# Performance work log

Measured on AMD Instinct MI355X. Metric: run time of the kernel, lower is better.

Reference implementation:

```python
import jax, jax.numpy as jnp
import numpy as np

N = 20000      # vertices
KPV = 8        # key points per vertex
M = N * KPV    # total key points
E = 320000     # edges (avg in-degree 16)
KP_DIM = 4
SD = 300       # state_dim
T = 3          # GNN iterations
NC = 4         # classes
LOC = (64, 64, 7)


def _lin(key, din, dout):
    k1, k2 = jax.random.split(key)
    s = 1.0 / np.sqrt(din)
    W = jax.random.uniform(k1, (din, dout), jnp.float32, -s, s)
    b = jax.random.uniform(k2, (dout,), jnp.float32, -s, s)
    return W, b


def setup_inputs():
    key = jax.random.key(0)
    ks = jax.random.split(key, 32)
    inp = {}
    inp['key_points'] = jax.random.normal(ks[0], (M, KP_DIM), jnp.float32)
    inp['pos'] = jax.random.normal(ks[1], (N, 3), jnp.float32)
    # uniform ragged layout: vertex i owns key points [i*KPV, (i+1)*KPV)
    inp['key_points_lookup'] = jnp.arange(N, dtype=jnp.int32) * KPV
    inp['edge_index'] = jax.random.randint(ks[2], (2, E), 0, N, jnp.int32)
    # MLPInit: kp_dim -> 64 -> 128 -> state_dim (basic_block = Linear+ReLU)
    inp['Wi0'], inp['bi0'] = _lin(ks[3], KP_DIM, 64)
    inp['Wi1'], inp['bi1'] = _lin(ks[4], 64, 128)
    inp['Wi2'], inp['bi2'] = _lin(ks[5], 128, SD)
    # MLPInitAggr: state_dim -> state_dim
    inp['Wa'], inp['ba'] = _lin(ks[6], SD, SD)
    # StateConvLayer params per iteration (mlp_h: s->delta_x, mlp_f: [dx,s_j]->e, mlp_g: update)
    Wh, bh, Wf, bf, Wg, bg = [], [], [], [], [], []
    for t in range(T):
        w, b = _lin(ks[7 + 3 * t], SD, 3); Wh.append(w); bh.append(b)
        w, b = _lin(ks[8 + 3 * t], SD + 3, SD); Wf.append(w); bf.append(b)
        w, b = _lin(ks[9 + 3 * t], SD, SD); Wg.append(w); bg.append(b)
    inp['Wh'] = jnp.stack(Wh); inp['bh'] = jnp.stack(bh)
    inp['Wf'] = jnp.stack(Wf); inp['bf'] = jnp.stack(bf)
    inp['Wg'] = jnp.stack(Wg); inp['bg'] = jnp.stack(bg)
    # classification head: state_dim -> 64 -> n_classes
    inp['Wc1'], inp['bc1'] = _lin(ks[16], SD, 64)
    inp['Wc2'], inp['bc2'] = _lin(ks[17], 64, NC)
    # per-class localization heads: state_dim -> 64 -> 64 -> 7 (stacked over classes)
    Wl1, bl1, Wl2, bl2, Wl3, bl3 = [], [], [], [], [], []
    for c in range(NC):
        w, b = _lin(ks[18 + 3 * c], SD, LOC[0]); Wl1.append(w); bl1.append(b)
        w, b = _lin(ks[19 + 3 * c], LOC[0], LOC[1]); Wl2.append(w); bl2.append(b)
        w, b = _lin(ks[20 + 3 * c], LOC[1], LOC[2]); Wl3.append(w); bl3.append(b)
    inp['Wl1'] = jnp.stack(Wl1); inp['bl1'] = jnp.stack(bl1)
    inp['Wl2'] = jnp.stack(Wl2); inp['bl2'] = jnp.stack(bl2)
    inp['Wl3'] = jnp.stack(Wl3); inp['bl3'] = jnp.stack(bl3)
    return inp


def reference(key_points, pos, key_points_lookup, edge_index,
              Wi0, bi0, Wi1, bi1, Wi2, bi2, Wa, ba,
              Wh, bh, Wf, bf, Wg, bg,
              Wc1, bc1, Wc2, bc2,
              Wl1, bl1, Wl2, bl2, Wl3, bl3):
    relu = jax.nn.relu
    n = pos.shape[0]
    # ---- initial vertex state: per-key-point MLP + ragged segment-max ----
    feats = relu(key_points @ Wi0 + bi0)
    feats = relu(feats @ Wi1 + bi1)
    feats = relu(feats @ Wi2 + bi2)                      # [M, SD]
    seg = jnp.searchsorted(key_points_lookup,
                           jnp.arange(feats.shape[0], dtype=jnp.int32),
                           side='right') - 1              # key point -> vertex id
    kp_max = jax.ops.segment_max(feats, seg, num_segments=n)  # [N, SD]
    s = relu(kp_max @ Wa + ba)                            # initial vertex states
    # ---- GNN iterations (Point-GNN eqns, max aggregation) ----
    src, dst = edge_index[0], edge_index[1]
    for t in range(Wh.shape[0]):
        dx = s @ Wh[t] + bh[t]                            # [N, 3] predicted offset
        m = jnp.concatenate([pos[src] - pos[dst] + dx[dst], s[src]], axis=-1)
        e = relu(m @ Wf[t] + bf[t])                       # [E, SD] edge messages
        aggr = jax.ops.segment_max(e, dst, num_segments=n)
        aggr = jnp.where(jnp.isneginf(aggr), 0.0, aggr)   # empty segments -> 0
        s = s + (aggr @ Wg[t] + bg[t])                    # residual state update
    # ---- heads ----
    cls_pred = relu(relu(s @ Wc1 + bc1) @ Wc2 + bc2)      # [N, NC]
    h = relu(jnp.einsum('nd,cdk->cnk', s, Wl1) + bl1[:, None, :])
    h = relu(jnp.einsum('cnd,cdk->cnk', h, Wl2) + bl2[:, None, :])
    h = relu(jnp.einsum('cnd,cdk->cnk', h, Wl3) + bl3[:, None, :])  # [C, N, 7]
    reg_pred = jnp.transpose(h, (1, 0, 2)).reshape(n, -1)           # [N, C*7]
    return cls_pred, reg_pred
```

## Files before the change

### kernel.cpp

```cpp
#include <hip/hip_runtime.h>
#include <stdint.h>

#define N_V   20000
#define M_KP  160000
#define E_N   320000
#define SD    300
#define T_IT  3

typedef unsigned short bf16_t;
typedef __attribute__((ext_vector_type(8))) short short8_t;
typedef __attribute__((ext_vector_type(4))) float float4_t;

__device__ __forceinline__ float bf2f(bf16_t u) {
    return __uint_as_float(((unsigned)u) << 16);
}
__device__ __forceinline__ bf16_t f2bf(float f) {
    unsigned u = __float_as_uint(f);
    unsigned r = (u + 0x7FFFu + ((u >> 16) & 1u)) >> 16;
    return (bf16_t)r;
}

template<bool F32>
__device__ __forceinline__ float LD(const void* p, size_t i) {
    if (F32) return ((const float*)p)[i];
    return bf2f(((const bf16_t*)p)[i]);
}
template<bool F32>
__device__ __forceinline__ void ST(void* p, size_t i, float v) {
    if (F32) ((float*)p)[i] = v;
    else     ((bf16_t*)p)[i] = f2bf(v);
}
__device__ __forceinline__ float LDr(const void* p, long long i, bool f32) {
    return f32 ? ((const float*)p)[i] : bf2f(((const bf16_t*)p)[i]);
}
__device__ __forceinline__ void STr(void* p, size_t i, float v, bool f32) {
    if (f32) ((float*)p)[i] = v;
    else     ((bf16_t*)p)[i] = f2bf(v);
}

__global__ void k_detect(const unsigned* __restrict__ w, int* __restrict__ flag) {
    __shared__ int cnt_s;
    if (threadIdx.x == 0) cnt_s = 0;
    __syncthreads();
    unsigned u = w[threadIdx.x];
    unsigned lo = u & 0xFFFFu;
    int e = (lo >> 7) & 0xFF;
    int plaus = (lo == 0u) || (e >= 96 && e <= 126);
    atomicAdd(&cnt_s, plaus);
    __syncthreads();
    if (threadIdx.x == 0) flag[0] = (cnt_s >= 64) ? 0 : 1;
}

__global__ void k_zero(int* p, int n) {
    int i = blockIdx.x * blockDim.x + threadIdx.x;
    if (i < n) p[i] = 0;
}
__global__ void k_hist(const int* __restrict__ dst, int* __restrict__ cnt) {
    int e = blockIdx.x * blockDim.x + threadIdx.x;
    if (e < E_N) atomicAdd(&cnt[dst[e]], 1);
}
__global__ void k_scan(const int* __restrict__ cnt, int* __restrict__ offs,
                       int* __restrict__ cur) {
    __shared__ int buf[1024];
    __shared__ int carry_s;
    int tid = threadIdx.x;
    if (tid == 0) { carry_s = 0; offs[0] = 0; }
    __syncthreads();
    for (int base = 0; base < N_V; base += 1024) {
        int i = base + tid;
        int v = (i < N_V) ? cnt[i] : 0;
        buf[tid] = v;
        __syncthreads();
        for (int off = 1; off < 1024; off <<= 1) {
            int t = (tid >= off) ? buf[tid - off] : 0;
            __syncthreads();
            buf[tid] += t;
            __syncthreads();
        }
        int incl = buf[tid] + carry_s;
        if (i < N_V) { offs[i + 1] = incl; cur[i] = incl - v; }
        __syncthreads();
        if (tid == 1023) carry_s = incl;
        __syncthreads();
    }
}
__global__ void k_scatter(const int* __restrict__ src, const int* __restrict__ dst,
                          int* __restrict__ cur, int* __restrict__ esrc) {
    int e = blockIdx.x * blockDim.x + threadIdx.x;
    if (e < E_N) {
        int p = atomicAdd(&cur[dst[e]], 1);
        esrc[p] = src[e];
    }
}

template<bool F32>
__global__ __launch_bounds__(256) void k_init_fused(
    const void* __restrict__ kp,
    const void* __restrict__ Wi0, const void* __restrict__ bi0,
    const void* __restrict__ Wi1, const void* __restrict__ bi1,
    const void* __restrict__ Wi2, const void* __restrict__ bi2,
    float* __restrict__ kpmax, const int* __restrict__ flag) {
    if ((flag[0] != 0) != F32) return;
    __shared__ float kps[256];
    __shared__ float h1s[64][64];
    __shared__ float h2s[64 * 128];
    int tid = threadIdx.x;
    int row0 = blockIdx.x * 64;
    kps[tid] = LD<F32>(kp, (size_t)row0 * 4 + tid);
    __syncthreads();
    {
        int c = tid & 63;
        float w0 = LD<F32>(Wi0, c), w1 = LD<F32>(Wi0, 64 + c);
        float w2 = LD<F32>(Wi0, 128 + c), w3 = LD<F32>(Wi0, 192 + c);
        float b0 = LD<F32>(bi0, c);
        int rbase = (tid >> 6) * 16;
#pragma unroll
        for (int rr = 0; rr < 16; rr++) {
            int r = rbase + rr;
            float a = b0 + kps[r * 4] * w0 + kps[r * 4 + 1] * w1
                         + kps[r * 4 + 2] * w2 + kps[r * 4 + 3] * w3;
            h1s[r][c] = fmaxf(a, 0.f);
        }
    }
    __syncthreads();
    {
        int c = tid & 127;
        int rbase = (tid >> 7) * 32;
        float b1 = LD<F32>(bi1, c);
        float acc[32];
#pragma unroll
        for (int rr = 0; rr < 32; rr++) acc[rr] = b1;
        for (int k = 0; k < 64; k++) {
            float wv = LD<F32>(Wi1, (size_t)k * 128 + c);
#pragma unroll
            for (int rr = 0; rr < 32; rr++) acc[rr] += h1s[rbase + rr][k] * wv;
        }
#pragma unroll
        for (int rr = 0; rr < 32; rr++)
            h2s[(size_t)(rbase + rr) * 128 + c] = fmaxf(acc[rr], 0.f);
    }
    __syncthreads();
    {
        int cx = tid & 63, rg = tid >> 6;
        float acc[16][5];
#pragma unroll
        for (int r = 0; r < 16; r++)
#pragma unroll
            for (int j = 0; j < 5; j++) acc[r][j] = 0.f;
        bool ok4 = (cx < SD - 256);
        for (int k = 0; k < 128; k++) {
            float w[5];
#pragma unroll
            for (int j = 0; j < 4; j++) w[j] = LD<F32>(Wi2, (size_t)k * SD + cx + 64 * j);
            w[4] = ok4 ? LD<F32>(Wi2, (size_t)k * SD + cx + 256) : 0.f;
#pragma unroll
            for (int r = 0; r < 16; r++) {
                float av = h2s[(rg * 16 + r) * 128 + k];
#pragma unroll
                for (int j = 0; j < 5; j++) acc[r][j] += av * w[j];
            }
        }
        int vbase = (row0 >> 3) + rg * 2;
#pragma unroll
        for (int half = 0; half < 2; half++) {
            int v = vbase + half;
#pragma unroll
            for (int j = 0; j < 5; j++) {
                int c = cx + 64 * j;
                if (c >= SD) continue;
                float m = acc[half * 8][j];
#pragma unroll
                for (int r = 1; r < 8; r++) m = fmaxf(m, acc[half * 8 + r][j]);
                kpmax[(size_t)v * SD + c] = fmaxf(m + LD<F32>(bi2, c), 0.f);
            }
        }
    }
}

template<bool F32>
__global__ __launch_bounds__(256) void k_gemm(
    const float* __restrict__ A, const void* __restrict__ W,
    const void* __restrict__ bias, const float* res,
    float* C, int Mr, int K, int Nc, int do_relu, const int* __restrict__ flag) {
    if ((flag[0] != 0) != F32) return;
    __shared__ float As[16][65];
    __shared__ float Ws[16][64];
    int tid = threadIdx.x;
    int tx = tid & 15, ty = tid >> 4;
    int row0 = blockIdx.y * 64, col0 = blockIdx.x * 64;
    float acc[4][4] = {{0.f}};
    int lk = tid & 15, lr = tid >> 4;
    int ln = tid & 63, lk4 = tid >> 6;
    for (int k0 = 0; k0 < K; k0 += 16) {
#pragma unroll
        for (int i = 0; i < 4; i++) {
            int r = lr + i * 16;
            int gr = row0 + r, gk = k0 + lk;
            As[lk][r] = (gr < Mr && gk < K) ? A[(size_t)gr * K + gk] : 0.f;
        }
#pragma unroll
        for (int p = 0; p < 4; p++) {
            int kk = lk4 + p * 4;
            int gk = k0 + kk, gn = col0 + ln;
            Ws[kk][ln] = (gk < K && gn < Nc) ? LD<F32>(W, (size_t)gk * Nc + gn) : 0.f;
        }
        __syncthreads();
#pragma unroll
        for (int kk = 0; kk < 16; kk++) {
            float a[4], w[4];
#pragma unroll
            for (int i = 0; i < 4; i++) a[i] = As[kk][ty * 4 + i];
#pragma unroll
            for (int j = 0; j < 4; j++) w[j] = Ws[kk][tx * 4 + j];
#pragma unroll
            for (int i = 0; i < 4; i++)
#pragma unroll
                for (int j = 0; j < 4; j++) acc[i][j] += a[i] * w[j];
        }
        __syncthreads();
    }
#pragma unroll
    for (int i = 0; i < 4; i++) {
        int gr = row0 + ty * 4 + i;
        if (gr >= Mr) continue;
#pragma unroll
        for (int j = 0; j < 4; j++) {
            int gn = col0 + tx * 4 + j;
            if (gn >= Nc) continue;
            float c = acc[i][j] + LD<F32>(bias, gn);
            if (res) c += res[(size_t)gr * Nc + gn];
            if (do_relu) c = fmaxf(c, 0.f);
            C[(size_t)gr * Nc + gn] = c;
        }
    }
}

#define PREP_SPLIT 882688
#define PREP_BIAS  3104
#define PREP_WF3   2700
#define PREP_TOT   (PREP_SPLIT + PREP_BIAS + PREP_WF3 + 32)

__global__ __launch_bounds__(256) void k_prep(
    const void* __restrict__ Wa, const void* __restrict__ Wf,
    const void* __restrict__ Wg, const void* __restrict__ Wc1,
    const void* __restrict__ Wl1, const void* __restrict__ Wl2,
    const void* __restrict__ Wi1, const void* __restrict__ Wi2,
    const void* __restrict__ ba, const void* __restrict__ bfb,
    const void* __restrict__ bgb, const void* __restrict__ bc1,
    const void* __restrict__ bl1b, const void* __restrict__ bl2b,
    const void* __restrict__ bi1, const void* __restrict__ bi2,
    unsigned short* __restrict__ SP, float* __restrict__ biasF,
    float* __restrict__ wf3F,
    float* __restrict__ bzero, const int* __restrict__ flag)
{
    int idx = blockIdx.x * 256 + threadIdx.x;
    if (idx >= PREP_TOT) return;
    bool f32 = flag[0] != 0;
    if (idx < PREP_SPLIT) {
        const void* src; long long eoff, cum; int srcN, Nn, Kk, Kpad, pe, local;
        if (idx < 716800) {
            int m = idx / 102400; local = idx - m * 102400;
            pe = 102400; cum = (long long)m * 102400;
            Kpad = 320; Nn = 300; Kk = 300; srcN = 300;
            src = (m == 0) ? Wa : (m <= 3 ? Wf : Wg);
            eoff = (m == 0) ? 0 : (m <= 3 ? (long long)((m - 1) * 303 + 3) * 300
                                          : (long long)(m - 4) * 90000);
        } else if (idx < 819200) {
            int j = (idx - 716800) / 20480; local = (idx - 716800) - j * 20480;
            pe = 20480; cum = 716800 + (long long)j * 20480;
            Kpad = 320; Nn = 64; Kk = 300; srcN = 64;
            src = (j == 0) ? Wc1 : Wl1;
            eoff = (j == 0) ? 0 : (long long)(j - 1) * 19200;
        } else if (idx < 835584) {
            int c = (idx - 819200) / 4096; local = (idx - 819200) - c * 4096;
            pe = 4096; cum = 819200 + (long long)c * 4096;
            Kpad = 64; Nn = 64; Kk = 64; srcN = 64;
            src = Wl2; eoff = (long long)c * 4096;
        } else if (idx < 843776) {
            local = idx - 835584;
            pe = 8192; cum = 835584;
            Kpad = 64; Nn = 128; Kk = 64; srcN = 128;
            src = Wi1; eoff = 0;
        } else {
            local = idx - 843776;
            pe = 38912; cum = 843776;
            Kpad = 128; Nn = 300; Kk = 128; srcN = 300;
            src = Wi2; eoff = 0;
        }
        int n = local / Kpad, k = local - n * Kpad;
        float v = 0.f;
        if (n < Nn && k < Kk) v = LDr(src, eoff + (long long)k * srcN + n, f32);
        bf16_t hi = f2bf(v);
        bf16_t lo = f2bf(v - bf2f(hi));
        SP[2 * cum + local] = hi;
        SP[2 * cum + pe + local] = lo;
    } else if (idx < PREP_SPLIT + PREP_BIAS) {
        int b = idx - PREP_SPLIT;
        const void* src; int o;
        if (b < 300)       { src = ba;   o = b; }
        else if (b < 1200) { src = bfb;  o = b - 300; }
        else if (b < 2100) { src = bgb;  o = b - 1200; }
        else if (b < 2164) { src = bc1;  o = b - 2100; }
        else if (b < 2420) { src = bl1b; o = b - 2164; }
        else if (b < 2676) { src = bl2b; o = b - 2420; }
        else if (b < 2804) { src = bi1;  o = b - 2676; }
        else               { src = bi2;  o = b - 2804; }
        biasF[b] = LDr(src, o, f32);
    } else if (idx < PREP_SPLIT + PREP_BIAS + PREP_WF3) {
        int b2 = idx - (PREP_SPLIT + PREP_BIAS);
        int t = b2 / 900, rem = b2 - t * 900;
        wf3F[b2] = LDr(Wf, (long long)t * 303 * SD + rem, f32);
    } else {
        bzero[idx - (PREP_SPLIT + PREP_BIAS + PREP_WF3)] = 0.f;
    }
}

__device__ __forceinline__ void mfma16(float4_t& c, short8_t a, short8_t b) {
    asm("v_mfma_f32_16x16x32_bf16 %0, %1, %2, %0" : "+v"(c) : "v"(a), "v"(b));
}
__device__ __forceinline__ void split2(float a, float b, unsigned& h, unsigned& l) {
    asm("v_cvt_pk_bf16_f32 %0, %1, %2" : "=v"(h) : "v"(a), "v"(b));
    float la = a - __uint_as_float(h << 16);
    float lb = b - __uint_as_float(h & 0xFFFF0000u);
    asm("v_cvt_pk_bf16_f32 %0, %1, %2" : "=v"(l) : "v"(la), "v"(lb));
}
__device__ __forceinline__ void split8(float4_t x0, float4_t x1,
                                       short8_t* hi, short8_t* lo) {
    union { unsigned u[4]; short8_t v; } H, L;
#pragma unroll
    for (int p = 0; p < 4; p++) {
        float a, b;
        if (p == 0)      { a = x0[0]; b = x0[1]; }
        else if (p == 1) { a = x0[2]; b = x0[3]; }
        else if (p == 2) { a = x1[0]; b = x1[1]; }
        else             { a = x1[2]; b = x1[3]; }
        unsigned ph, pl;
        split2(a, b, ph, pl);
        H.u[p] = ph; L.u[p] = pl;
    }
    *hi = H.v; *lo = L.v;
}

__global__ __launch_bounds__(256) void k_init_mfma(
    const void* __restrict__ kp,
    const void* __restrict__ Wi0, const void* __restrict__ bi0,
    const unsigned short* __restrict__ W1T,
    const unsigned short* __restrict__ W2T,
    const float* __restrict__ b1F, const float* __restrict__ b2F,
    float* __restrict__ kpmax, const int* __restrict__ flag)
{
    bool f32 = flag[0] != 0;
    __shared__ __attribute__((aligned(16))) unsigned short lds[2][8704];
    int tid = threadIdx.x;
    int w = tid >> 6, lane = tid & 63;
    int rg = w >> 1, ch = w & 1;
    int l15 = lane & 15, g = lane >> 4;
    unsigned short* h2h = lds[rg];
    unsigned short* h2l = lds[rg] + 4352;
    int rw0 = blockIdx.x * 64 + rg * 32;

    float kpr[2][4];
#pragma unroll
    for (int mt = 0; mt < 2; mt++) {
        long long r = rw0 + mt * 16 + l15;
#pragma unroll
        for (int j = 0; j < 4; j++) kpr[mt][j] = LDr(kp, r * 4 + j, f32);
    }
    short8_t a1h[2][2], a1l[2][2];
#pragma unroll
    for (int ks = 0; ks < 2; ks++) {
        float h[2][8];
#pragma unroll
        for (int e = 0; e < 8; e++) {
            int chn = ks * 32 + 8 * g + e;
            float w0 = LDr(Wi0, chn, f32),       w1 = LDr(Wi0, 64 + chn, f32);
            float w2 = LDr(Wi0, 128 + chn, f32), w3 = LDr(Wi0, 192 + chn, f32);
            float b0 = LDr(bi0, chn, f32);
#pragma unroll
            for (int mt = 0; mt < 2; mt++)
                h[mt][e] = fmaxf(b0 + kpr[mt][0] * w0 + kpr[mt][1] * w1
                                    + kpr[mt][2] * w2 + kpr[mt][3] * w3, 0.f);
        }
#pragma unroll
        for (int mt = 0; mt < 2; mt++) {
            union { unsigned u[4]; short8_t v; } H, L;
#pragma unroll
            for (int p = 0; p < 4; p++) {
                unsigned hh, ll;
                split2(h[mt][2 * p], h[mt][2 * p + 1], hh, ll);
                H.u[p] = hh; L.u[p] = ll;
            }
            a1h[mt][ks] = H.v; a1l[mt][ks] = L.v;
        }
    }

#pragma unroll
    for (int i = 0; i < 4; i++) {
        int n0 = ch * 4 + i;
        const unsigned short* bp = W1T + (n0 * 16 + l15) * 64 + 8 * g;
        short8_t bh0 = *(const short8_t*)bp;
        short8_t bh1 = *(const short8_t*)(bp + 32);
        short8_t bl0 = *(const short8_t*)(bp + 8192);
        short8_t bl1 = *(const short8_t*)(bp + 8224);
        float4_t c0 = {0.f, 0.f, 0.f, 0.f}, c1 = {0.f, 0.f, 0.f, 0.f};
        mfma16(c0, a1h[0][0], bh0); mfma16(c0, a1h[0][1], bh1);
        mfma16(c0, a1l[0][0], bh0); mfma16(c0, a1l[0][1], bh1);
        mfma16(c0, a1h[0][0], bl0); mfma16(c0, a1h[0][1], bl1);
        mfma16(c1, a1h[1][0], bh0); mfma16(c1, a1h[1][1], bh1);
        mfma16(c1, a1l[1][0], bh0); mfma16(c1, a1l[1][1], bh1);
        mfma16(c1, a1h[1][0], bl0); mfma16(c1, a1h[1][1], bl1);
        int col = n0 * 16 + l15;
        float bv = b1F[col];
#pragma unroll
        for (int i2 = 0; i2 < 4; i2++) {
            float v0 = fmaxf(c0[i2] + bv, 0.f);
            bf16_t h0 = f2bf(v0);
            h2h[(4 * g + i2) * 136 + col] = h0;
            h2l[(4 * g + i2) * 136 + col] = f2bf(v0 - bf2f(h0));
            float v1 = fmaxf(c1[i2] + bv, 0.f);
            bf16_t h1v = f2bf(v1);
            h2h[(16 + 4 * g + i2) * 136 + col] = h1v;
            h2l[(16 + 4 * g + i2) * 136 + col] = f2bf(v1 - bf2f(h1v));
        }
    }
    __syncthreads();

    short8_t a2h[2][4], a2l[2][4];
#pragma unroll
    for (int mt = 0; mt < 2; mt++)
#pragma unroll
        for (int ks = 0; ks < 4; ks++) {
            int off = (mt * 16 + l15) * 136 + ks * 32 + 8 * g;
            a2h[mt][ks] = *(const short8_t*)(h2h + off);
            a2l[mt][ks] = *(const short8_t*)(h2l + off);
        }
    int vb = blockIdx.x * 8 + rg * 4;
    int n0beg = ch ? 10 : 0, n0end = ch ? 19 : 10;
    for (int n0 = n0beg; n0 < n0end; n0++) {
        const unsigned short* bp = W2T + (n0 * 16 + l15) * 128 + 8 * g;
        short8_t bh[4], bl[4];
#pragma unroll
        for (int ks = 0; ks < 4; ks++) {
            bh[ks] = *(const short8_t*)(bp + ks * 32);
            bl[ks] = *(const short8_t*)(bp + 38912 + ks * 32);
        }
        float4_t c0 = {0.f, 0.f, 0.f, 0.f}, c1 = {0.f, 0.f, 0.f, 0.f};
#pragma unroll
        for (int ks = 0; ks < 4; ks++) {
            mfma16(c0, a2h[0][ks], bh[ks]); mfma16(c1, a2h[1][ks], bh[ks]);
        }
#pragma unroll
        for (int ks = 0; ks < 4; ks++) {
            mfma16(c0, a2l[0][ks], bh[ks]); mfma16(c1, a2l[1][ks], bh[ks]);
        }
#pragma unroll
        for (int ks = 0; ks < 4; ks++) {
            mfma16(c0, a2h[0][ks], bl[ks]); mfma16(c1, a2h[1][ks], bl[ks]);
        }
        float m0 = fmaxf(fmaxf(c0[0], c0[1]), fmaxf(c0[2], c0[3]));
        m0 = fmaxf(m0, __shfl_xor(m0, 16));
        float m1 = fmaxf(fmaxf(c1[0], c1[1]), fmaxf(c1[2], c1[3]));
        m1 = fmaxf(m1, __shfl_xor(m1, 16));
        int col = n0 * 16 + l15;
        if (col < SD) {
            float bv = b2F[col];
            if (g == 0) {
                kpmax[(size_t)(vb + 0) * SD + col] = fmaxf(m0 + bv, 0.f);
                kpmax[(size_t)(vb + 2) * SD + col] = fmaxf(m1 + bv, 0.f);
            } else if (g == 2) {
                kpmax[(size_t)(vb + 1) * SD + col] = fmaxf(m0 + bv, 0.f);
                kpmax[(size_t)(vb + 3) * SD + col] = fmaxf(m1 + bv, 0.f);
            }
        }
    }
}

__global__ __launch_bounds__(256) void k_gemm_mfma(
    const float* __restrict__ A, const unsigned short* __restrict__ WhiT,
    const unsigned short* __restrict__ WloT, const float* __restrict__ bias,
    const float* __restrict__ res, float* __restrict__ C,
    int M, int K, int Kpad, int N, int relu,
    long long zA, long long zW, int zB, long long zC,
    const void* posp, const float* dxv, const float* wf3F,
    float* bbag, const int* __restrict__ flag)
{
    int z = blockIdx.z;
    A    += (size_t)z * zA;
    WhiT += (size_t)z * zW;
    WloT += (size_t)z * zW;
    bias += (size_t)z * zB;
    C    += (size_t)z * zC;
    int tid = threadIdx.x;
    int w = tid >> 6, lane = tid & 63;
    int l15 = lane & 15, g = lane >> 4;
    int row0 = blockIdx.y * 256 + w * 64;
    int col0 = blockIdx.x * 64;

    float4_t acc[4][4];
#pragma unroll
    for (int i = 0; i < 4; i++)
#pragma unroll
        for (int j = 0; j < 4; j++) acc[i][j] = (float4_t){0.f, 0.f, 0.f, 0.f};

    const unsigned short* bhp[4];
    const unsigned short* blp[4];
#pragma unroll
    for (int ns = 0; ns < 4; ns++) {
        size_t o = (size_t)(col0 + ns * 16 + l15) * Kpad + 8 * g;
        bhp[ns] = WhiT + o; blp[ns] = WloT + o;
    }
    const float* app[4];
    int amode[4]; bool adead[4];
#pragma unroll
    for (int ms = 0; ms < 4; ms++) {
        int base = row0 + ms * 16;
        int gr = base + l15;
        amode[ms] = (base + 16 <= M) ? 2 : (base < M ? 1 : 0);
        adead[ms] = gr >= M;
        int grc = gr < M ? gr : (M - 1);
        app[ms] = A + (size_t)grc * K + 8 * g;
    }
    const short8_t z8 = {0, 0, 0, 0, 0, 0, 0, 0};

    for (int k0 = 0; k0 < K; k0 += 32) {
        short8_t bh[4], bl[4], ah[4], al[4];
#pragma unroll
        for (int ns = 0; ns < 4; ns++) {
            bh[ns] = *(const short8_t*)bhp[ns]; bhp[ns] += 32;
            bl[ns] = *(const short8_t*)blp[ns]; blp[ns] += 32;
        }
#pragma unroll
        for (int ms = 0; ms < 4; ms++) {
            if (amode[ms] == 0) { ah[ms] = z8; al[ms] = z8; continue; }
            float4_t x0 = *(const float4_t*)app[ms];
            float4_t x1 = *(const float4_t*)(app[ms] + 4);
            app[ms] += 32;
            if (amode[ms] == 1 && adead[ms]) {
                x0 = (float4_t){0.f, 0.f, 0.f, 0.f};
                x1 = (float4_t){0.f, 0.f, 0.f, 0.f};
            }
            split8(x0, x1, &ah[ms], &al[ms]);
        }
#pragma unroll
        for (int ms = 0; ms < 4; ms++)
#pragma unroll
            for (int ns = 0; ns < 4; ns++) {
                mfma16(acc[ms][ns], ah[ms], bh[ns]);
                mfma16(acc[ms][ns], al[ms], bh[ns]);
                mfma16(acc[ms][ns], ah[ms], bl[ns]);
            }
    }

    bool ab = posp != nullptr;
    bool pf32 = ab && (flag[0] != 0);
#pragma unroll
    for (int ns = 0; ns < 4; ns++) {
        int gn = col0 + ns * 16 + l15;
        if (gn >= N) continue;
        float bv = bias[gn];
        float w30 = 0.f, w31 = 0.f, w32 = 0.f;
        if (ab) { w30 = wf3F[gn]; w31 = wf3F[300 + gn]; w32 = wf3F[600 + gn]; }
#pragma unroll
        for (int ms = 0; ms < 4; ms++) {
            int rb = row0 + ms * 16 + 4 * g;
#pragma unroll
            for (int r = 0; r < 4; r++) {
                int gr = rb + r;
                if (gr >= M) continue;
                float c = acc[ms][ns][r] + bv;
                if (ab) {
                    float P = LDr(posp, (long long)gr * 3 + 0, pf32) * w30
                            + LDr(posp, (long long)gr * 3 + 1, pf32) * w31
                            + LDr(posp, (long long)gr * 3 + 2, pf32) * w32;
                    float D = dxv[gr * 3 + 0] * w30 + dxv[gr * 3 + 1] * w31
                            + dxv[gr * 3 + 2] * w32;
                    c += P;
                    bbag[(size_t)gr * N + gn] = D - P;
                }
                if (res) c += res[(size_t)gr * N + gn];
                if (relu) c = fmaxf(c, 0.f);
                C[(size_t)gr * N + gn] = c;
            }
        }
    }
}

__global__ void k_dx2(const float* __restrict__ s, const void* __restrict__ Wh,
                      const void* __restrict__ bh, int t, float* __restrict__ dx,
                      const int* __restrict__ flag) {
    bool f32 = flag[0] != 0;
    long long wo = (long long)t * SD * 3, bo = (long long)t * 3;
    int wv = threadIdx.x >> 6, lane = threadIdx.x & 63;
    int v = blockIdx.x * 4 + wv;
    if (v >= N_V) return;
    float p0 = 0.f, p1 = 0.f, p2 = 0.f;
    for (int d = lane; d < SD; d += 64) {
        float sv = s[(size_t)v * SD + d];
        p0 += sv * LDr(Wh, wo + d * 3 + 0, f32);
        p1 += sv * LDr(Wh, wo + d * 3 + 1, f32);
        p2 += sv * LDr(Wh, wo + d * 3 + 2, f32);
    }
#pragma unroll
    for (int off = 32; off > 0; off >>= 1) {
        p0 += __shfl_down(p0, off);
        p1 += __shfl_down(p1, off);
        p2 += __shfl_down(p2, off);
    }
    if (lane == 0) {
        dx[v * 3 + 0] = p0 + LDr(bh, bo + 0, f32);
        dx[v * 3 + 1] = p1 + LDr(bh, bo + 1, f32);
        dx[v * 3 + 2] = p2 + LDr(bh, bo + 2, f32);
    }
}

__global__ void k_cls2(const float* __restrict__ hc, const void* __restrict__ W,
                       const void* __restrict__ b, void* __restrict__ out,
                       const int* __restrict__ flag) {
    bool f32 = flag[0] != 0;
    int v = blockIdx.x * blockDim.x + threadIdx.x;
    if (v >= N_V) return;
    float acc[4];
#pragma unroll
    for (int j = 0; j < 4; j++) acc[j] = LDr(b, j, f32);
    for (int k = 0; k < 64; k++) {
        float h = hc[(size_t)v * 64 + k];
#pragma unroll
        for (int j = 0; j < 4; j++) acc[j] += h * LDr(W, k * 4 + j, f32);
    }
#pragma unroll
    for (int j = 0; j < 4; j++) STr(out, v * 4 + j, fmaxf(acc[j], 0.f), f32);
}

__global__ void k_loc32(const float* __restrict__ hl2all, const void* __restrict__ Wl3,
                        const void* __restrict__ bl3, void* __restrict__ out,
                        const int* __restrict__ flag) {
    bool f32 = flag[0] != 0;
    int cls = blockIdx.y;
    const float* h2 = hl2all + (size_t)cls * N_V * 64;
    long long wo = (long long)cls * 64 * 7, bo = (long long)cls * 7;
    int v = blockIdx.x * blockDim.x + threadIdx.x;
    if (v >= N_V) return;
    float acc[7];
#pragma unroll
    for (int j = 0; j < 7; j++) acc[j] = LDr(bl3, bo + j, f32);
    for (int k = 0; k < 64; k++) {
        float h = h2[(size_t)v * 64 + k];
#pragma unroll
        for (int j = 0; j < 7; j++) acc[j] += h * LDr(Wl3, wo + k * 7 + j, f32);
    }
#pragma unroll
    for (int j = 0; j < 7; j++)
        STr(out, 80000 + (size_t)v * 28 + cls * 7 + j, fmaxf(acc[j], 0.f), f32);
}

template<bool F32>
__global__ void k_dx(const float* __restrict__ s, const void* __restrict__ Wh,
                     const void* __restrict__ bh, float* __restrict__ dx,
                     const int* __restrict__ flag) {
    if ((flag[0] != 0) != F32) return;
    int wv = threadIdx.x >> 6, lane = threadIdx.x & 63;
    int v = blockIdx.x * 4 + wv;
    if (v >= N_V) return;
    float p0 = 0.f, p1 = 0.f, p2 = 0.f;
    for (int d = lane; d < SD; d += 64) {
        float sv = s[(size_t)v * SD + d];
        p0 += sv * LD<F32>(Wh, d * 3 + 0);
        p1 += sv * LD<F32>(Wh, d * 3 + 1);
        p2 += sv * LD<F32>(Wh, d * 3 + 2);
    }
#pragma unroll
    for (int off = 32; off > 0; off >>= 1) {
        p0 += __shfl_down(p0, off);
        p1 += __shfl_down(p1, off);
        p2 += __shfl_down(p2, off);
    }
    if (lane == 0) {
        dx[v * 3 + 0] = p0 + LD<F32>(bh, 0);
        dx[v * 3 + 1] = p1 + LD<F32>(bh, 1);
        dx[v * 3 + 2] = p2 + LD<F32>(bh, 2);
    }
}

template<bool F32>
__global__ void k_ab(const float* __restrict__ dx, const void* __restrict__ pos,
                     const void* __restrict__ Wf3, float* __restrict__ ua,
                     float* __restrict__ bbag, const int* __restrict__ flag) {
    if ((flag[0] != 0) != F32) return;
    int idx = blockIdx.x * blockDim.x + threadIdx.x;
    if (idx >= N_V * SD) return;
    int v = idx / SD, c = idx - v * SD;
    float w0 = LD<F32>(Wf3, c), w1 = LD<F32>(Wf3, SD + c), w2 = LD<F32>(Wf3, 2 * SD + c);
    float P = LD<F32>(pos, v * 3 + 0) * w0 + LD<F32>(pos, v * 3 + 1) * w1
            + LD<F32>(pos, v * 3 + 2) * w2;
    float D = dx[v * 3 + 0] * w0 + dx[v * 3 + 1] * w1 + dx[v * 3 + 2] * w2;
    ua[idx] += P;
    bbag[idx] = D - P;
}

__global__ __launch_bounds__(256) void k_aggr(
    const float* __restrict__ a, float* bbag,
    const int* __restrict__ offs, const int* __restrict__ esrc) {
    int wv = threadIdx.x >> 6, lane = threadIdx.x & 63;
    int v = blockIdx.x * 4 + wv;
    if (v >= N_V) return;
    int e0 = offs[v], e1 = offs[v + 1];
    float r0 = -3.0e38f, r1 = r0, r2 = r0, r3 = r0, r4 = r0;
    bool c4 = lane < SD - 256;
    for (int e = e0; e < e1; e++) {
        const float* ar = a + (size_t)esrc[e] * SD + lane;
        r0 = fmaxf(r0, ar[0]);
        r1 = fmaxf(r1, ar[64]);
        r2 = fmaxf(r2, ar[128]);
        r3 = fmaxf(r3, ar[192]);
        if (c4) r4 = fmaxf(r4, ar[256]);
    }
    float* bv = bbag + (size_t)v * SD + lane;
    bv[0]   = fmaxf(0.f, r0 + bv[0]);
    bv[64]  = fmaxf(0.f, r1 + bv[64]);
    bv[128] = fmaxf(0.f, r2 + bv[128]);
    bv[192] = fmaxf(0.f, r3 + bv[192]);
    if (c4) bv[256] = fmaxf(0.f, r4 + bv[256]);
}

template<bool F32>
__global__ void k_cls(const float* __restrict__ hc, const void* __restrict__ W,
                      const void* __restrict__ b, void* __restrict__ out,
                      const int* __restrict__ flag) {
    if ((flag[0] != 0) != F32) return;
    int v = blockIdx.x * blockDim.x + threadIdx.x;
    if (v >= N_V) return;
    float acc[4];
#pragma unroll
    for (int j = 0; j < 4; j++) acc[j] = LD<F32>(b, j);
    for (int k = 0; k < 64; k++) {
        float h = hc[(size_t)v * 64 + k];
#pragma unroll
        for (int j = 0; j < 4; j++) acc[j] += h * LD<F32>(W, k * 4 + j);
    }
#pragma unroll
    for (int j = 0; j < 4; j++) ST<F32>(out, v * 4 + j, fmaxf(acc[j], 0.f));
}

template<bool F32>
__global__ void k_loc3(const float* __restrict__ h2, const void* __restrict__ W,
                       const void* __restrict__ b, void* __restrict__ out, int cls,
                       const int* __restrict__ flag) {
    if ((flag[0] != 0) != F32) return;
    int v = blockIdx.x * blockDim.x + threadIdx.x;
    if (v >= N_V) return;
    float acc[7];
#pragma unroll
    for (int j = 0; j < 7; j++) acc[j] = LD<F32>(b, j);
    for (int k = 0; k < 64; k++) {
        float h = h2[(size_t)v * 64 + k];
#pragma unroll
        for (int j = 0; j < 7; j++) acc[j] += h * LD<F32>(W, k * 7 + j);
    }
#pragma unroll
    for (int j = 0; j < 7; j++)
        ST<F32>(out, 80000 + (size_t)v * 28 + cls * 7 + j, fmaxf(acc[j], 0.f));
}

#define LAUNCH2(kname, grid, blk, ...) \
    do { kname<false><<<grid, blk, 0, stream>>>(__VA_ARGS__); \
         kname<true><<<grid, blk, 0, stream>>>(__VA_ARGS__); } while (0)

extern "C" void kernel_launch(void* const* d_in, const int* in_sizes, int n_in,
                              void* d_out, int out_size, void* d_ws, size_t ws_size,
                              hipStream_t stream) {
    const void* kp  = d_in[0];
    const void* pos = d_in[1];
    const int* eidx = (const int*)d_in[3];
    const int* e_src = eidx;
    const int* e_dst = eidx + E_N;
    const void* Wi0 = d_in[4];   const void* bi0 = d_in[5];
    const void* Wi1 = d_in[6];   const void* bi1 = d_in[7];
    const void* Wi2 = d_in[8];   const void* bi2 = d_in[9];
    const void* Wa  = d_in[10];  const void* ba  = d_in[11];
    const char* Wh  = (const char*)d_in[12];  const char* bh = (const char*)d_in[13];
    const char* Wf  = (const char*)d_in[14];  const char* bff = (const char*)d_in[15];
    const char* Wg  = (const char*)d_in[16];  const char* bg = (const char*)d_in[17];
    const void* Wc1 = d_in[18];  const void* bc1 = d_in[19];
    const void* Wc2 = d_in[20];  const void* bc2 = d_in[21];
    const char* Wl1 = (const char*)d_in[22];  const char* bl1 = (const char*)d_in[23];
    const char* Wl2 = (const char*)d_in[24];  const char* bl2 = (const char*)d_in[25];
    const char* Wl3 = (const char*)d_in[26];  const char* bl3 = (const char*)d_in[27];

    char* ws = (char*)d_ws;
    float* regA  = (float*)(ws + 0);
    float* kpmax = regA;
    float* ua    = regA;
    float* hc    = (float*)(ws + 0);
    float* hl1m  = (float*)(ws + 0);
    float* hl1f  = (float*)(ws + 6000000);
    float* hl2f  = (float*)(ws + 12000000);
    float* bbag  = (float*)(ws + 24000000);
    float* hl2m  = (float*)(ws + 24000000);
    float* s     = (float*)(ws + 48000000);
    int*   cnt   = (int*)(ws + 72000000);
    int*   offs  = (int*)(ws + 72100000);
    int*   cur   = (int*)(ws + 72200000);
    int*   esrc  = (int*)(ws + 72300000);
    float* dx    = (float*)(ws + 73600000);
    float* wf3F  = (float*)(ws + 73844000);
    int*   flag  = (int*)(ws + 73900000);
    unsigned short* SPLIT = (unsigned short*)(ws + 73950000);
    float* biasF = (float*)(ws + 77481000);

    bool mf = (ws_size == 0) || (ws_size >= (size_t)77500000);
    auto HI = [&](long long cum) { return SPLIT + 2 * cum; };

    k_detect<<<1, 128, 0, stream>>>((const unsigned*)Wi0, flag);

    k_zero<<<(N_V + 255) / 256, 256, 0, stream>>>(cnt, N_V);
    k_hist<<<(E_N + 255) / 256, 256, 0, stream>>>(e_dst, cnt);
    k_scan<<<1, 1024, 0, stream>>>(cnt, offs, cur);
    k_scatter<<<(E_N + 255) / 256, 256, 0, stream>>>(e_src, e_dst, cur, esrc);

    if (mf)
        k_prep<<<(PREP_TOT + 255) / 256, 256, 0, stream>>>(
            Wa, Wf, Wg, Wc1, Wl1, Wl2, Wi1, Wi2,
            ba, bff, bg, bc1, bl1, bl2, bi1, bi2,
            SPLIT, biasF, wf3F, bbag, flag);

    if (mf) {
        const unsigned short* W1T = SPLIT + 2LL * 835584;
        const unsigned short* W2T = SPLIT + 2LL * 843776;
        k_init_mfma<<<M_KP / 64, 256, 0, stream>>>(kp, Wi0, bi0, W1T, W2T,
                                                   biasF + 2676, biasF + 2804,
                                                   kpmax, flag);
    } else {
        LAUNCH2(k_init_fused, M_KP / 64, 256, kp, Wi0, bi0, Wi1, bi1, Wi2, bi2, kpmax, flag);
    }

    const dim3 GSD(5, (N_V + 255) / 256);
    const dim3 G64(1, (N_V + 255) / 256);
    if (mf) {
        k_gemm_mfma<<<GSD, 256, 0, stream>>>(kpmax, HI(0), HI(0) + 102400,
                                             biasF, nullptr, s, N_V, SD, 320, SD, 1,
                                             0, 0, 0, 0,
                                             nullptr, nullptr, nullptr, nullptr, nullptr);
    } else {
        dim3 g((SD + 63) / 64, (N_V + 63) / 64);
        LAUNCH2(k_gemm, g, 256, kpmax, Wa, ba, nullptr, s, N_V, SD, SD, 1, flag);
    }

    for (int t = 0; t < T_IT; t++) {
        dim3 g5((SD + 63) / 64, (N_V + 63) / 64);
        if (mf) {
            k_dx2<<<(N_V + 3) / 4, 256, 0, stream>>>(s, Wh, bh, t, dx, flag);
            long long cum = (long long)(1 + t) * 102400;
            k_gemm_mfma<<<GSD, 256, 0, stream>>>(s, HI(cum), HI(cum) + 102400,
                                                 biasF + 300 + t * 300, nullptr, ua,
                                                 N_V, SD, 320, SD, 0, 0, 0, 0, 0,
                                                 pos, dx, wf3F + t * 900, bbag, flag);
        } else {
            for (int f32v = 0; f32v < 2; f32v++) {
                size_t es = f32v ? 4 : 2;
                const void* Wf_t = Wf + (size_t)t * 303 * SD * es;
                const void* WfS  = Wf + ((size_t)t * 303 + 3) * SD * es;
                const void* bf_t = bff + (size_t)t * SD * es;
                const void* Wh_t = Wh + (size_t)t * SD * 3 * es;
                const void* bh_t = bh + (size_t)t * 3 * es;
                if (f32v) {
                    k_gemm<true><<<g5, 256, 0, stream>>>(s, WfS, bf_t, nullptr, ua, N_V, SD, SD, 0, flag);
                    k_dx<true><<<(N_V + 3) / 4, 256, 0, stream>>>(s, Wh_t, bh_t, dx, flag);
                    k_ab<true><<<(N_V * SD + 255) / 256, 256, 0, stream>>>(dx, pos, Wf_t, ua, bbag, flag);
                } else {
                    k_gemm<false><<<g5, 256, 0, stream>>>(s, WfS, bf_t, nullptr, ua, N_V, SD, SD, 0, flag);
                    k_dx<false><<<(N_V + 3) / 4, 256, 0, stream>>>(s, Wh_t, bh_t, dx, flag);
                    k_ab<false><<<(N_V * SD + 255) / 256, 256, 0, stream>>>(dx, pos, Wf_t, ua, bbag, flag);
                }
            }
        }
        k_aggr<<<(N_V + 3) / 4, 256, 0, stream>>>(ua, bbag, offs, esrc);
        if (mf) {
            long long cum = (long long)(4 + t) * 102400;
            k_gemm_mfma<<<GSD, 256, 0, stream>>>(bbag, HI(cum), HI(cum) + 102400,
                                                 biasF + 1200 + t * 300, s, s,
                                                 N_V, SD, 320, SD, 0, 0, 0, 0, 0,
                                                 nullptr, nullptr, nullptr, nullptr, nullptr);
        } else {
            for (int f32v = 0; f32v < 2; f32v++) {
                size_t es = f32v ? 4 : 2;
                const void* Wg_t = Wg + (size_t)t * SD * SD * es;
                const void* bg_t = bg + (size_t)t * SD * es;
                if (f32v)
                    k_gemm<true><<<g5, 256, 0, stream>>>(bbag, Wg_t, bg_t, s, s, N_V, SD, SD, 0, flag);
                else
                    k_gemm<false><<<g5, 256, 0, stream>>>(bbag, Wg_t, bg_t, s, s, N_V, SD, SD, 0, flag);
            }
        }
    }

    if (mf) {
        k_gemm_mfma<<<G64, 256, 0, stream>>>(s, HI(716800), HI(716800) + 20480,
                                             biasF + 2100, nullptr, hc,
                                             N_V, SD, 320, 64, 1, 0, 0, 0, 0,
                                             nullptr, nullptr, nullptr, nullptr, nullptr);
        k_cls2<<<(N_V + 255) / 256, 256, 0, stream>>>(hc, Wc2, bc2, d_out, flag);
        dim3 gz1(1, (N_V + 255) / 256, 4);
        k_gemm_mfma<<<gz1, 256, 0, stream>>>(s, HI(737280), HI(737280) + 20480,
                                             biasF + 2164, nullptr, hl1m,
                                             N_V, SD, 320, 64, 1,
                                             0, 40960, 64, 1280000,
                                             nullptr, nullptr, nullptr, nullptr, nullptr);
        k_gemm_mfma<<<gz1, 256, 0, stream>>>(hl1m, HI(819200), HI(819200) + 4096,
                                             biasF + 2420, nullptr, hl2m,
                                             N_V, 64, 64, 64, 1,
                                             1280000, 8192, 64, 1280000,
                                             nullptr, nullptr, nullptr, nullptr, nullptr);
        dim3 gz3((N_V + 255) / 256, 4);
        k_loc32<<<gz3, 256, 0, stream>>>(hl2m, Wl3, bl3, d_out, flag);
    } else {
        dim3 g(1, (N_V + 63) / 64);
        LAUNCH2(k_gemm, g, 256, s, Wc1, bc1, nullptr, hc, N_V, SD, 64, 1, flag);
        LAUNCH2(k_cls, (N_V + 255) / 256, 256, hc, Wc2, bc2, d_out, flag);
        for (int c = 0; c < 4; c++) {
            for (int f32v = 0; f32v < 2; f32v++) {
                size_t es = f32v ? 4 : 2;
                const void* Wl1c = Wl1 + (size_t)c * SD * 64 * es;
                const void* bl1c = bl1 + (size_t)c * 64 * es;
                const void* Wl2c = Wl2 + (size_t)c * 64 * 64 * es;
                const void* bl2c = bl2 + (size_t)c * 64 * es;
                const void* Wl3c = Wl3 + (size_t)c * 64 * 7 * es;
                const void* bl3c = bl3 + (size_t)c * 7 * es;
                if (f32v) {
                    k_gemm<true><<<g, 256, 0, stream>>>(s, Wl1c, bl1c, nullptr, hl1f, N_V, SD, 64, 1, flag);
                    k_gemm<true><<<g, 256, 0, stream>>>(hl1f, Wl2c, bl2c, nullptr, hl2f, N_V, 64, 64, 1, flag);
                    k_loc3<true><<<(N_V + 255) / 256, 256, 0, stream>>>(hl2f, Wl3c, bl3c, d_out, c, flag);
                } else {
                    k_gemm<false><<<g, 256, 0, stream>>>(s, Wl1c, bl1c, nullptr, hl1f, N_V, SD, 64, 1, flag);
                    k_gemm<false><<<g, 256, 0, stream>>>(hl1f, Wl2c, bl2c, nullptr, hl2f, N_V, 64, 64, 1, flag);
                    k_loc3<false><<<(N_V + 255) / 256, 256, 0, stream>>>(hl2f, Wl3c, bl3c, d_out, c, flag);
                }
            }
        }
    }
}
```

Baseline: 1.190 ms.

## Halve MFMA GEMM row tile and double-buffer register loads across K steps

Each block of the split-bf16 MFMA GEMM now covers 128 rows instead of 256, with each wave owning 32 rows. This roughly doubles the number of blocks for better CU coverage and cuts accumulator register use. The K loop is restructured into a two-stage register ping-pong so the next slice's A and B loads are issued before the current slice's MFMAs. The epilogue loads pos and dx once per row rather than once per column. The costs are more B-operand reloads across blocks, and the ping-pong loop assumes an even iteration count.

```diff
diff --git a/kernel.cpp b/kernel.cpp
--- a/kernel.cpp
+++ b/kernel.cpp
@@ -493,12 +493,12 @@
     int tid = threadIdx.x;
     int w = tid >> 6, lane = tid & 63;
     int l15 = lane & 15, g = lane >> 4;
-    int row0 = blockIdx.y * 256 + w * 64;
+    int row0 = blockIdx.y * 128 + w * 32;
     int col0 = blockIdx.x * 64;
 
-    float4_t acc[4][4];
-#pragma unroll
-    for (int i = 0; i < 4; i++)
+    float4_t acc[2][4];
+#pragma unroll
+    for (int i = 0; i < 2; i++)
 #pragma unroll
         for (int j = 0; j < 4; j++) acc[i][j] = (float4_t){0.f, 0.f, 0.f, 0.f};
 
@@ -509,10 +509,10 @@
         size_t o = (size_t)(col0 + ns * 16 + l15) * Kpad + 8 * g;
         bhp[ns] = WhiT + o; blp[ns] = WloT + o;
     }
-    const float* app[4];
-    int amode[4]; bool adead[4];
-#pragma unroll
-    for (int ms = 0; ms < 4; ms++) {
+    const float* app[2];
+    int amode[2]; bool adead[2];
+#pragma unroll
+    for (int ms = 0; ms < 2; ms++) {
         int base = row0 + ms * 16;
         int gr = base + l15;
         amode[ms] = (base + 16 <= M) ? 2 : (base < M ? 1 : 0);
@@ -520,60 +520,87 @@
         int grc = gr < M ? gr : (M - 1);
         app[ms] = A + (size_t)grc * K + 8 * g;
     }
-    const short8_t z8 = {0, 0, 0, 0, 0, 0, 0, 0};
-
-    for (int k0 = 0; k0 < K; k0 += 32) {
-        short8_t bh[4], bl[4], ah[4], al[4];
+    const float4_t zf4 = {0.f, 0.f, 0.f, 0.f};
+
+    auto LOADB = [&](short8_t* bh, short8_t* bl) {
 #pragma unroll
         for (int ns = 0; ns < 4; ns++) {
-            bh[ns] = *(const short8_t*)bhp[ns]; bhp[ns] += 32;
-            bl[ns] = *(const short8_t*)blp[ns]; blp[ns] += 32;
-        }
-#pragma unroll
-        for (int ms = 0; ms < 4; ms++) {
-            if (amode[ms] == 0) { ah[ms] = z8; al[ms] = z8; continue; }
-            float4_t x0 = *(const float4_t*)app[ms];
-            float4_t x1 = *(const float4_t*)(app[ms] + 4);
+            bh[ns] = *(const short8_t*)bhp[ns];
+            bl[ns] = *(const short8_t*)blp[ns];
+            bhp[ns] += 32; blp[ns] += 32;
+        }
+    };
+    auto LOADA = [&](float4_t* x0, float4_t* x1) {
+#pragma unroll
+        for (int ms = 0; ms < 2; ms++) {
+            if (amode[ms] == 0) { x0[ms] = zf4; x1[ms] = zf4; }
+            else {
+                x0[ms] = *(const float4_t*)app[ms];
+                x1[ms] = *(const float4_t*)(app[ms] + 4);
+                if (amode[ms] == 1 && adead[ms]) { x0[ms] = zf4; x1[ms] = zf4; }
+            }
             app[ms] += 32;
-            if (amode[ms] == 1 && adead[ms]) {
-                x0 = (float4_t){0.f, 0.f, 0.f, 0.f};
-                x1 = (float4_t){0.f, 0.f, 0.f, 0.f};
-            }
-            split8(x0, x1, &ah[ms], &al[ms]);
-        }
-#pragma unroll
-        for (int ms = 0; ms < 4; ms++)
+        }
+    };
+    auto COMPUTE = [&](const short8_t* bh, const short8_t* bl,
+                       const float4_t* x0, const float4_t* x1) {
+#pragma unroll
+        for (int ms = 0; ms < 2; ms++) {
+            short8_t ah, al;
+            split8(x0[ms], x1[ms], &ah, &al);
 #pragma unroll
             for (int ns = 0; ns < 4; ns++) {
-                mfma16(acc[ms][ns], ah[ms], bh[ns]);
-                mfma16(acc[ms][ns], al[ms], bh[ns]);
-                mfma16(acc[ms][ns], ah[ms], bl[ns]);
-            }
+                mfma16(acc[ms][ns], ah, bh[ns]);
+                mfma16(acc[ms][ns], al, bh[ns]);
+                mfma16(acc[ms][ns], ah, bl[ns]);
+            }
+        }
+    };
+
+    short8_t bhA[4], blA[4], bhB[4], blB[4];
+    float4_t x0A[2], x1A[2], x0B[2], x1B[2];
+    int iters = (K + 31) / 32;
+    LOADB(bhA, blA); LOADA(x0A, x1A);
+    for (int it = 0; it < iters; it += 2) {
+        LOADB(bhB, blB); LOADA(x0B, x1B);
+        COMPUTE(bhA, blA, x0A, x1A);
+        if (it + 2 < iters) { LOADB(bhA, blA); LOADA(x0A, x1A); }
+        COMPUTE(bhB, blB, x0B, x1B);
     }
 
     bool ab = posp != nullptr;
     bool pf32 = ab && (flag[0] != 0);
+    int gnv[4]; float bvv[4], w30v[4], w31v[4], w32v[4];
 #pragma unroll
     for (int ns = 0; ns < 4; ns++) {
         int gn = col0 + ns * 16 + l15;
-        if (gn >= N) continue;
-        float bv = bias[gn];
-        float w30 = 0.f, w31 = 0.f, w32 = 0.f;
-        if (ab) { w30 = wf3F[gn]; w31 = wf3F[300 + gn]; w32 = wf3F[600 + gn]; }
-#pragma unroll
-        for (int ms = 0; ms < 4; ms++) {
-            int rb = row0 + ms * 16 + 4 * g;
-#pragma unroll
-            for (int r = 0; r < 4; r++) {
-                int gr = rb + r;
-                if (gr >= M) continue;
-                float c = acc[ms][ns][r] + bv;
+        gnv[ns] = gn;
+        bvv[ns] = (gn < N) ? bias[gn] : 0.f;
+        if (ab && gn < N) {
+            w30v[ns] = wf3F[gn]; w31v[ns] = wf3F[300 + gn]; w32v[ns] = wf3F[600 + gn];
+        } else { w30v[ns] = 0.f; w31v[ns] = 0.f; w32v[ns] = 0.f; }
+    }
+#pragma unroll
+    for (int ms = 0; ms < 2; ms++) {
+#pragma unroll
+        for (int r = 0; r < 4; r++) {
+            int gr = row0 + ms * 16 + 4 * g + r;
+            if (gr >= M) continue;
+            float p0 = 0.f, p1 = 0.f, p2 = 0.f, d0 = 0.f, d1 = 0.f, d2 = 0.f;
+            if (ab) {
+                p0 = LDr(posp, (long long)gr * 3 + 0, pf32);
+                p1 = LDr(posp, (long long)gr * 3 + 1, pf32);
+                p2 = LDr(posp, (long long)gr * 3 + 2, pf32);
+                d0 = dxv[gr * 3 + 0]; d1 = dxv[gr * 3 + 1]; d2 = dxv[gr * 3 + 2];
+            }
+#pragma unroll
+            for (int ns = 0; ns < 4; ns++) {
+                int gn = gnv[ns];
+                if (gn >= N) continue;
+                float c = acc[ms][ns][r] + bvv[ns];
                 if (ab) {
-                    float P = LDr(posp, (long long)gr * 3 + 0, pf32) * w30
-                            + LDr(posp, (long long)gr * 3 + 1, pf32) * w31
-                            + LDr(posp, (long long)gr * 3 + 2, pf32) * w32;
-                    float D = dxv[gr * 3 + 0] * w30 + dxv[gr * 3 + 1] * w31
-                            + dxv[gr * 3 + 2] * w32;
+                    float P = p0 * w30v[ns] + p1 * w31v[ns] + p2 * w32v[ns];
+                    float D = d0 * w30v[ns] + d1 * w31v[ns] + d2 * w32v[ns];
                     c += P;
                     bbag[(size_t)gr * N + gn] = D - P;
                 }
@@ -833,8 +860,8 @@
         LAUNCH2(k_init_fused, M_KP / 64, 256, kp, Wi0, bi0, Wi1, bi1, Wi2, bi2, kpmax, flag);
     }
 
-    const dim3 GSD(5, (N_V + 255) / 256);
-    const dim3 G64(1, (N_V + 255) / 256);
+    const dim3 GSD(5, (N_V + 127) / 128);
+    const dim3 G64(1, (N_V + 127) / 128);
     if (mf) {
         k_gemm_mfma<<<GSD, 256, 0, stream>>>(kpmax, HI(0), HI(0) + 102400,
                                              biasF, nullptr, s, N_V, SD, 320, SD, 1,
@@ -899,7 +926,7 @@
                                              N_V, SD, 320, 64, 1, 0, 0, 0, 0,
                                              nullptr, nullptr, nullptr, nullptr, nullptr);
         k_cls2<<<(N_V + 255) / 256, 256, 0, stream>>>(hc, Wc2, bc2, d_out, flag);
-        dim3 gz1(1, (N_V + 255) / 256, 4);
+        dim3 gz1(1, (N_V + 127) / 128, 4);
         k_gemm_mfma<<<gz1, 256, 0, stream>>>(s, HI(737280), HI(737280) + 20480,
                                              biasF + 2164, nullptr, hl1m,
                                              N_V, SD, 320, 64, 1,
```

After: 1.182 ms. Within noise of the previous version (-0.7%).
